# Optimization experiments

Hardware: AMD Instinct MI355X
Metric: run time of the kernel (lower is better)

Reference implementation:

```python
import jax, jax.numpy as jnp
import numpy as np

SCALE = 2
K_UP = 5
K_ENC = 3


def _conv(x, w, b, pad):
    # NCHW conv, OIHW weights
    y = jax.lax.conv_general_dilated(
        x, w, window_strides=(1, 1), padding=((pad, pad), (pad, pad)),
        dimension_numbers=('NCHW', 'OIHW', 'NCHW'))
    return y + b[None, :, None, None]


def setup_inputs() -> dict:
    key = jax.random.key(0)
    k0, k1, k2 = jax.random.split(key, 3)
    b, c, h, w = 4, 256, 64, 64
    c_mid = 64
    n_kernel = SCALE * SCALE * K_UP * K_UP  # 100
    x = jax.random.normal(k0, (b, c, h, w), jnp.float32)
    w1 = jax.random.normal(k1, (c_mid, c, K_ENC, K_ENC), jnp.float32) * 0.02
    b1 = jnp.zeros((c_mid,), jnp.float32)
    w2 = jax.random.normal(k2, (n_kernel, c_mid, 1, 1), jnp.float32) * 0.02
    b2 = jnp.zeros((n_kernel,), jnp.float32)
    return {"x": x, "w1": w1, "b1": b1, "w2": w2, "b2": b2}


def reference(x, w1, b1, w2, b2):
    b, c, h, w = x.shape
    s, k = SCALE, K_UP
    # kernel prediction encoder: 3x3 conv -> ReLU -> 1x1 conv
    feat = jax.nn.relu(_conv(x, w1, b1, K_ENC // 2))
    kern = _conv(feat, w2, b2, 0)                     # (b, s^2*k^2, h, w)
    kern = jax.nn.softmax(kern, axis=1)               # softmax over full channel dim (as in source)
    kern = kern.reshape(b, s * s, k * k, h, w)
    # F.unfold(x, k, padding=k//2) -> (b, c, k^2, h, w); torch ordering: kh major, kw minor
    pad = k // 2
    xp = jnp.pad(x, ((0, 0), (0, 0), (pad, pad), (pad, pad)))
    patches = jnp.stack([xp[:, :, i:i + h, j:j + w]
                         for i in range(k) for j in range(k)], axis=2)  # (b, c, k^2, h, w)
    # per-pixel weighted reassembly: sum over k^2 neighborhood
    out = jnp.einsum('bskhw,bckhw->bschw', kern, patches)  # (b, s^2, c, h, w)
    # view(b, s^2*c, h, w) then pixel_shuffle(scale), exactly matching torch semantics
    out = out.reshape(b, s * s * c, h, w)
    cout = (s * s * c) // (s * s)
    out = out.reshape(b, cout, s, s, h, w)
    out = out.transpose(0, 1, 4, 2, 5, 3).reshape(b, cout, h * s, w * s)
    return out
```

## Files before the change

### kernel.cpp

```cpp
#include <hip/hip_runtime.h>


#define BB 4
#define CC 256
#define HH 64
#define WW 64
#define CMID 64
#define NKCH 100

typedef __bf16 bf16;
typedef __bf16 bf16x8 __attribute__((ext_vector_type(8)));
typedef float f32x4 __attribute__((ext_vector_type(4)));

__device__ __forceinline__ void async_copy16(const void* gsrc, void* ldst) {
    __builtin_amdgcn_global_load_lds(
        (__attribute__((address_space(1))) void*)(void*)gsrc,
        (__attribute__((address_space(3))) void*)ldst, 16, 0, 0);
}

__global__ void k0a_transform(const float* __restrict__ w1, bf16* __restrict__ w1c) {
    int c8 = blockIdx.x;
    int oq = blockIdx.y;
    int tid = threadIdx.x;
    __shared__ __align__(16) float wf[16 * 300];

    for (int i = tid; i < 16 * 72; i += 256) {
        int o = i / 72, r = i % 72;
        *(float4*)&wf[o * 300 + r * 4] =
            *(const float4*)&w1[(size_t)(oq * 16 + o) * 2304 + c8 * 288 + r * 4];
    }
    __syncthreads();

    for (int t = tid; t < 576; t += 256) {
        int o = t & 15, q = (t >> 4) & 3, kk = t >> 6;
        union { bf16 h[8]; uint4 u; } v;
        #pragma unroll
        for (int i8 = 0; i8 < 8; ++i8)
            v.h[i8] = (bf16)wf[o * 300 + (q * 8 + i8) * 9 + kk];
        *(uint4*)&w1c[(size_t)((((c8 * 9 + kk) * 4 + q) * 64) + oq * 16 + o) * 8] = v.u;
    }
}

__global__ __launch_bounds__(512) void k12_fused(const float* __restrict__ x,
        const bf16* __restrict__ w1c, const float* __restrict__ b1,
        const float* __restrict__ w2, const float* __restrict__ b2,
        float* __restrict__ kern) {
    int bh = blockIdx.x;
    int b = bh >> 6, h = bh & 63;
    int tid = threadIdx.x;
    int lane = tid & 63, wid = tid >> 6;
    int l15 = lane & 15, quad = lane >> 4;
    int mhalf = wid & 1, nq = wid >> 1;

    __shared__ __align__(16) char smem[122112];
    bf16*  xs0  = (bf16*)smem;
    bf16*  xs1  = (bf16*)(smem + 15872);
    bf16*  wl0  = (bf16*)(smem + 31744);
    bf16*  wl1  = (bf16*)(smem + 68608);
    float* fs   = (float*)(smem + 105472);
    float* kts  = (float*)(smem + 31744);
    float* red  = (float*)smem;

    const float* xb = x + (size_t)b * (CC * HH * WW);

    int ppp[6], rrr[6];
    bool vmask[6];
    #pragma unroll
    for (int j = 0; j < 6; ++j) {
        int task = wid + j * 8;
        ppp[j] = task & 15;
        rrr[j] = task >> 4;
        int hr = h - 1 + rrr[j];
        vmask[j] = (hr >= 0 && hr < HH);
    }

    float fA0[6], fA1[6], fB0[6], fB1[6];
    #define LOADX(C8, F0, F1)                                                    \
        _Pragma("unroll")                                                        \
        for (int j = 0; j < 6; ++j) {                                            \
            if (vmask[j]) {                                                      \
                const float* src = xb + ((size_t)((C8) * 32 + 2 * ppp[j]) * (HH * WW)) \
                                 + (h - 1 + rrr[j]) * WW + lane;                 \
                F0[j] = src[0]; F1[j] = src[HH * WW];                            \
            }                                                                    \
        }
    #define WRITEB(F0, F1, XSDST)                                                \
        _Pragma("unroll")                                                        \
        for (int j = 0; j < 6; ++j) {                                            \
            if (vmask[j]) {                                                      \
                union { bf16 hh[2]; unsigned u; } cv;                            \
                cv.hh[0] = (bf16)F0[j]; cv.hh[1] = (bf16)F1[j];                  \
                *(unsigned*)&XSDST[(rrr[j] * 66 + 1 + lane) * 40 + 2 * ppp[j]] = cv.u; \
            }                                                                    \
        }
    #define ACOPY(C8, WDST)                                                      \
        for (int t = wid; t < 36; t += 8)                                        \
            async_copy16(w1c + ((((C8) * 36 + t) << 9) + lane * 8), (void*)&WDST[t << 9]);
    #define MFMAS(XSRC, WSRC)                                                    \
        _Pragma("unroll")                                                        \
        for (int kk = 0; kk < 9; ++kk) {                                         \
            int r3 = kk / 3, kw = kk % 3;                                        \
            bf16x8 a0 = *(const bf16x8*)&WSRC[((kk * 4 + quad) * 64 + mhalf * 32 + l15) * 8]; \
            bf16x8 a1 = *(const bf16x8*)&WSRC[((kk * 4 + quad) * 64 + mhalf * 32 + 16 + l15) * 8]; \
            bf16x8 xv = *(const bf16x8*)&XSRC[(r3 * 66 + nq * 16 + l15 + kw) * 40 + quad * 8]; \
            acc0 = __builtin_amdgcn_mfma_f32_16x16x32_bf16(a0, xv, acc0, 0, 0, 0); \
            acc1 = __builtin_amdgcn_mfma_f32_16x16x32_bf16(a1, xv, acc1, 0, 0, 0); \
        }

    for (int i = tid; i < 7936; i += 512) { xs0[i] = (bf16)0.f; xs1[i] = (bf16)0.f; }
    LOADX(0, fA0, fA1)
    ACOPY(0, wl0)
    __syncthreads();
    WRITEB(fA0, fA1, xs0)
    LOADX(1, fB0, fB1)
    __syncthreads();

    f32x4 acc0 = {0.f, 0.f, 0.f, 0.f}, acc1 = {0.f, 0.f, 0.f, 0.f};

    for (int c8 = 0; c8 < 8; c8 += 2) {
        ACOPY(c8 + 1, wl1)
        MFMAS(xs0, wl0)
        WRITEB(fB0, fB1, xs1)
        if (c8 < 6) { LOADX(c8 + 2, fA0, fA1) }
        __syncthreads();
        if (c8 < 6) { ACOPY(c8 + 2, wl0) }
        MFMAS(xs1, wl1)
        if (c8 < 6) { WRITEB(fA0, fA1, xs0) }
        if (c8 < 6) { LOADX(c8 + 3, fB0, fB1) }
        __syncthreads();
    }

    int px = nq * 16 + l15;
    #pragma unroll
    for (int mi = 0; mi < 2; ++mi) {
        int oc0 = mhalf * 32 + mi * 16 + quad * 4;
        float4 bv = *(const float4*)&b1[oc0];
        f32x4 v = mi ? acc1 : acc0;
        fs[(oc0 + 0) * 65 + px] = fmaxf(v[0] + bv.x, 0.f);
        fs[(oc0 + 1) * 65 + px] = fmaxf(v[1] + bv.y, 0.f);
        fs[(oc0 + 2) * 65 + px] = fmaxf(v[2] + bv.z, 0.f);
        fs[(oc0 + 3) * 65 + px] = fmaxf(v[3] + bv.w, 0.f);
    }
    __syncthreads();

    int w = lane;
    int g = wid, s2 = g & 3, ihalf = g >> 2;
    int i0 = ihalf ? 13 : 0;

    float4 fv[16];
    #pragma unroll
    for (int q = 0; q < 16; ++q) {
        fv[q].x = fs[(4 * q + 0) * 65 + w];
        fv[q].y = fs[(4 * q + 1) * 65 + w];
        fv[q].z = fs[(4 * q + 2) * 65 + w];
        fv[q].w = fs[(4 * q + 3) * 65 + w];
    }

    float lg[13];
    #pragma unroll
    for (int ii = 0; ii < 13; ++ii) {
        int idx = i0 + ii;
        bool act = (idx < 25);
        int oc = s2 * 25 + (act ? idx : 0);
        float a = b2[oc];
        const float4* wr = (const float4*)&w2[oc * 64];
        #pragma unroll
        for (int q = 0; q < 16; ++q) {
            float4 wv = wr[q];
            a += fv[q].x * wv.x + fv[q].y * wv.y + fv[q].z * wv.z + fv[q].w * wv.w;
        }
        lg[ii] = act ? a : -1e30f;
    }

    float m = -1e30f;
    #pragma unroll
    for (int ii = 0; ii < 13; ++ii) m = fmaxf(m, lg[ii]);
    red[g * 64 + w] = m;
    __syncthreads();
    m = fmaxf(fmaxf(fmaxf(red[0 * 64 + w], red[1 * 64 + w]),
                    fmaxf(red[2 * 64 + w], red[3 * 64 + w])),
              fmaxf(fmaxf(red[4 * 64 + w], red[5 * 64 + w]),
                    fmaxf(red[6 * 64 + w], red[7 * 64 + w])));
    float ssum = 0.f;
    #pragma unroll
    for (int ii = 0; ii < 13; ++ii) { lg[ii] = __expf(lg[ii] - m); ssum += lg[ii]; }
    red[512 + g * 64 + w] = ssum;
    __syncthreads();
    ssum = ((red[512 + 0 * 64 + w] + red[512 + 1 * 64 + w]) +
            (red[512 + 2 * 64 + w] + red[512 + 3 * 64 + w])) +
           ((red[512 + 4 * 64 + w] + red[512 + 5 * 64 + w]) +
            (red[512 + 6 * 64 + w] + red[512 + 7 * 64 + w]));
    float inv = 1.f / ssum;
    #pragma unroll
    for (int ii = 0; ii < 13; ++ii)
        if (i0 + ii < 25) kts[((i0 + ii) * 64 + w) * 4 + s2] = lg[ii] * inv;
    __syncthreads();

    float* kout = kern + (size_t)bh * 6400;
    for (int i = tid; i < 1600; i += 512)
        *(float4*)&kout[i * 4] = *(const float4*)&kts[i * 4];
    #undef LOADX
    #undef WRITEB
    #undef ACOPY
    #undef MFMAS
}

__global__ __launch_bounds__(256, 6) void k3_reassemble(const float* __restrict__ x,
        const float* __restrict__ kern, float* __restrict__ out) {
    int chunk = blockIdx.x;
    int bh = blockIdx.y;
    int b = bh >> 6, h = bh & 63;
    int tid = threadIdx.x;
    int w = tid & 63;
    int cg = tid >> 6;

    __shared__ __align__(16) float xs[5 * 4 * 68 * 4];

    #pragma unroll
    for (int k = 0; k < 5; ++k) {
        int idx = tid + k * 256;
        int u = idx & 15, cc = (idx >> 4) & 15, rr = idx >> 8;
        int hr = h - 2 + rr;
        float4 v = make_float4(0.f, 0.f, 0.f, 0.f);
        if (hr >= 0 && hr < HH)
            v = *(const float4*)&x[(((size_t)b * CC + chunk * 16 + cc) * HH + hr) * WW + 4 * u];
        int base = (rr * 4 + (cc >> 2)) * 68;
        int c = cc & 3;
        #pragma unroll
        for (int j = 0; j < 4; ++j) {
            int s = 2 + 4 * u + j;
            int sw = s ^ ((s >> 3) & 7);
            xs[(base + sw) * 4 + c] = ((const float*)&v)[j];
        }
    }
    for (int i = tid; i < 320; i += 256) {
        int c = i & 3;
        int q = (i >> 2) & 3;
        int rg = i >> 4;
        int slot = (q < 2) ? q : (q + 64);
        xs[(rg * 68 + slot) * 4 + c] = 0.f;
    }

    const float* kp = kern + (size_t)bh * 6400 + w * 4;
    f32x4 kv0[5];
    #pragma unroll
    for (int kw = 0; kw < 5; ++kw)
        kv0[kw] = *(const f32x4*)&kp[kw * 256];

    int swk[5];
    #pragma unroll
    for (int kw = 0; kw < 5; ++kw) {
        int s = w + kw;
        swk[kw] = s ^ ((s >> 3) & 7);
    }

    __syncthreads();

    f32x4 a0 = {0.f,0.f,0.f,0.f}, a1 = {0.f,0.f,0.f,0.f};
    f32x4 a2 = {0.f,0.f,0.f,0.f}, a3 = {0.f,0.f,0.f,0.f};
    #pragma unroll
    for (int r = 0; r < 5; ++r) {
        #pragma unroll
        for (int kw = 0; kw < 5; ++kw) {
            f32x4 kv = (r == 0) ? kv0[kw]
                                : *(const f32x4*)&kp[(r * 5 + kw) * 256];
            f32x4 xv = *(const f32x4*)&xs[((r * 4 + cg) * 68 + swk[kw]) * 4];
            a0 += kv.x * xv;
            a1 += kv.y * xv;
            a2 += kv.z * xv;
            a3 += kv.w * xv;
        }
    }

    int cq = chunk * 4 + cg;
    f32x4 accs[4] = {a0, a1, a2, a3};
    #pragma unroll
    for (int s = 0; s < 4; ++s) {
        size_t base = (((size_t)b * 256 + s * 64 + cq) * 128 + 2 * h) * 128 + 2 * w;
        *(float2*)&out[base]       = make_float2(accs[s][0], accs[s][1]);
        *(float2*)&out[base + 128] = make_float2(accs[s][2], accs[s][3]);
    }
}

extern "C" void kernel_launch(void* const* d_in, const int* in_sizes, int n_in,
                              void* d_out, int out_size, void* d_ws, size_t ws_size,
                              hipStream_t stream) {
    const float* x  = (const float*)d_in[0];
    const float* w1 = (const float*)d_in[1];
    const float* b1 = (const float*)d_in[2];
    const float* w2 = (const float*)d_in[3];
    const float* b2 = (const float*)d_in[4];
    float* out = (float*)d_out;

    char* wsb = (char*)d_ws;
    float* kern = (float*)wsb;
    bf16*  w1c  = (bf16*)(wsb + 6553600);

    k0a_transform<<<dim3(8, 4), 256, 0, stream>>>(w1, w1c);
    k12_fused<<<dim3(BB * HH), 512, 0, stream>>>(x, w1c, b1, w2, b2, kern);
    k3_reassemble<<<dim3(16, BB * HH), 256, 0, stream>>>(x, kern, out);
}
```

Before: 132.6 us.

## Fuse reassembly into encoder kernel, keeping softmax kernels in registers

Merges the reassembly stage into the encoder/softmax kernel. Each block now keeps its row's 100 softmax weights in registers from LDS instead of writing them to a global workspace and reading them back. The block then loops over 8 channel chunks, double-buffering x tiles in LDS while it computes. This removes a kernel launch and the workspace round trip. The cost is only 256 blocks of 512 threads handling all 256 channels, so parallelism and occupancy drop compared with the 4096-block reassembly grid.

```diff
diff --git a/kernel.cpp b/kernel.cpp
--- a/kernel.cpp
+++ b/kernel.cpp
@@ -41,10 +41,10 @@
     }
 }
 
-__global__ __launch_bounds__(512) void k12_fused(const float* __restrict__ x,
+__global__ __launch_bounds__(512) void k123_fused(const float* __restrict__ x,
         const bf16* __restrict__ w1c, const float* __restrict__ b1,
         const float* __restrict__ w2, const float* __restrict__ b2,
-        float* __restrict__ kern) {
+        float* __restrict__ out) {
     int bh = blockIdx.x;
     int b = bh >> 6, h = bh & 63;
     int tid = threadIdx.x;
@@ -58,7 +58,7 @@
     bf16*  wl0  = (bf16*)(smem + 31744);
     bf16*  wl1  = (bf16*)(smem + 68608);
     float* fs   = (float*)(smem + 105472);
-    float* kts  = (float*)(smem + 31744);
+    float* kts  = (float*)(smem + 68608);
     float* red  = (float*)smem;
 
     const float* xb = x + (size_t)b * (CC * HH * WW);
@@ -90,19 +90,19 @@
             if (vmask[j]) {                                                      \
                 union { bf16 hh[2]; unsigned u; } cv;                            \
                 cv.hh[0] = (bf16)F0[j]; cv.hh[1] = (bf16)F1[j];                  \
-                *(unsigned*)&XSDST[(rrr[j] * 66 + 1 + lane) * 40 + 2 * ppp[j]] = cv.u; \
+                *(unsigned*)&(XSDST)[(rrr[j] * 66 + 1 + lane) * 40 + 2 * ppp[j]] = cv.u; \
             }                                                                    \
         }
     #define ACOPY(C8, WDST)                                                      \
         for (int t = wid; t < 36; t += 8)                                        \
-            async_copy16(w1c + ((((C8) * 36 + t) << 9) + lane * 8), (void*)&WDST[t << 9]);
+            async_copy16(w1c + ((((C8) * 36 + t) << 9) + lane * 8), (void*)&(WDST)[t << 9]);
     #define MFMAS(XSRC, WSRC)                                                    \
         _Pragma("unroll")                                                        \
         for (int kk = 0; kk < 9; ++kk) {                                         \
             int r3 = kk / 3, kw = kk % 3;                                        \
-            bf16x8 a0 = *(const bf16x8*)&WSRC[((kk * 4 + quad) * 64 + mhalf * 32 + l15) * 8]; \
-            bf16x8 a1 = *(const bf16x8*)&WSRC[((kk * 4 + quad) * 64 + mhalf * 32 + 16 + l15) * 8]; \
-            bf16x8 xv = *(const bf16x8*)&XSRC[(r3 * 66 + nq * 16 + l15 + kw) * 40 + quad * 8]; \
+            bf16x8 a0 = *(const bf16x8*)&(WSRC)[((kk * 4 + quad) * 64 + mhalf * 32 + l15) * 8]; \
+            bf16x8 a1 = *(const bf16x8*)&(WSRC)[((kk * 4 + quad) * 64 + mhalf * 32 + 16 + l15) * 8]; \
+            bf16x8 xv = *(const bf16x8*)&(XSRC)[(r3 * 66 + nq * 16 + l15 + kw) * 40 + quad * 8]; \
             acc0 = __builtin_amdgcn_mfma_f32_16x16x32_bf16(a0, xv, acc0, 0, 0, 0); \
             acc1 = __builtin_amdgcn_mfma_f32_16x16x32_bf16(a1, xv, acc1, 0, 0, 0); \
         }
@@ -143,6 +143,35 @@
     }
     __syncthreads();
 
+    int t8 = tid & 255, h2 = tid >> 8;
+    int w3 = t8 & 63, cg3 = t8 >> 6;
+    #define XLOAD(P, V)                                                          \
+        _Pragma("unroll")                                                        \
+        for (int k = 0; k < 5; ++k) {                                            \
+            int idx = t8 + k * 256;                                              \
+            int u = idx & 15, cc = (idx >> 4) & 15, rr = idx >> 8;               \
+            int hr = h - 2 + rr;                                                 \
+            V[k] = make_float4(0.f, 0.f, 0.f, 0.f);                              \
+            if (hr >= 0 && hr < HH)                                              \
+                V[k] = *(const float4*)&x[(((size_t)b * CC + (2 * (P) + h2) * 16 + cc) * HH + hr) * WW + 4 * u]; \
+        }
+    #define XWRITE(V, TB)                                                        \
+        _Pragma("unroll")                                                        \
+        for (int k = 0; k < 5; ++k) {                                            \
+            int idx = t8 + k * 256;                                              \
+            int u = idx & 15, cc = (idx >> 4) & 15, rr = idx >> 8;               \
+            int bse = (rr * 4 + (cc >> 2)) * 68;                                 \
+            int c = cc & 3;                                                      \
+            _Pragma("unroll")                                                    \
+            for (int j = 0; j < 4; ++j) {                                        \
+                int s = 2 + 4 * u + j;                                           \
+                int sw = s ^ ((s >> 3) & 7);                                     \
+                (TB)[(bse + sw) * 4 + c] = ((const float*)&V[k])[j];             \
+            }                                                                    \
+        }
+    float4 xst[5];
+    XLOAD(0, xst)
+
     int w = lane;
     int g = wid, s2 = g & 3, ihalf = g >> 2;
     int i0 = ihalf ? 13 : 0;
@@ -196,90 +225,73 @@
         if (i0 + ii < 25) kts[((i0 + ii) * 64 + w) * 4 + s2] = lg[ii] * inv;
     __syncthreads();
 
-    float* kout = kern + (size_t)bh * 6400;
-    for (int i = tid; i < 1600; i += 512)
-        *(float4*)&kout[i * 4] = *(const float4*)&kts[i * 4];
+    f32x4 kv[5][5];
+    #pragma unroll
+    for (int r = 0; r < 5; ++r)
+        #pragma unroll
+        for (int kw = 0; kw < 5; ++kw)
+            kv[r][kw] = *(const f32x4*)&kts[((r * 5 + kw) * 64 + w3) * 4];
+
+    #pragma unroll
+    for (int reg = 0; reg < 4; ++reg) {
+        const int tb = (reg == 0) ? 0 : (reg == 1) ? 21760 : (reg == 2) ? 43520 : 94208;
+        if (tid < 320) {
+            int c = tid & 3, q = (tid >> 2) & 3, rg = tid >> 4;
+            int slot = (q < 2) ? q : (q + 64);
+            ((float*)(smem + tb))[(rg * 68 + slot) * 4 + c] = 0.f;
+        }
+    }
+
+    float* tb0 = (float*)(smem + (h2 ? 21760 : 0));
+    float* tb1 = (float*)(smem + (h2 ? 94208 : 43520));
+
+    int swk[5];
+    #pragma unroll
+    for (int kw = 0; kw < 5; ++kw) {
+        int s = w3 + kw;
+        swk[kw] = s ^ ((s >> 3) & 7);
+    }
+
+    XWRITE(xst, tb0)
+    __syncthreads();
+
+    for (int p = 0; p < 8; ++p) {
+        if (p < 7) { XLOAD(p + 1, xst) }
+        float* T = (p & 1) ? tb1 : tb0;
+        f32x4 a0 = {0.f,0.f,0.f,0.f}, a1 = {0.f,0.f,0.f,0.f};
+        f32x4 a2 = {0.f,0.f,0.f,0.f}, a3 = {0.f,0.f,0.f,0.f};
+        #pragma unroll
+        for (int r = 0; r < 5; ++r) {
+            #pragma unroll
+            for (int kw = 0; kw < 5; ++kw) {
+                f32x4 kvv = kv[r][kw];
+                f32x4 xv = *(const f32x4*)&T[((r * 4 + cg3) * 68 + swk[kw]) * 4];
+                a0 += kvv.x * xv;
+                a1 += kvv.y * xv;
+                a2 += kvv.z * xv;
+                a3 += kvv.w * xv;
+            }
+        }
+        int cq = (2 * p + h2) * 4 + cg3;
+        f32x4 accs[4] = {a0, a1, a2, a3};
+        #pragma unroll
+        for (int s = 0; s < 4; ++s) {
+            size_t base = (((size_t)b * 256 + s * 64 + cq) * 128 + 2 * h) * 128 + 2 * w3;
+            *(float2*)&out[base]       = make_float2(accs[s][0], accs[s][1]);
+            *(float2*)&out[base + 128] = make_float2(accs[s][2], accs[s][3]);
+        }
+        if (p < 7) {
+            float* Tnext = (p & 1) ? tb0 : tb1;
+            XWRITE(xst, Tnext)
+        }
+        __syncthreads();
+    }
     #undef LOADX
     #undef WRITEB
     #undef ACOPY
     #undef MFMAS
-}
-
-__global__ __launch_bounds__(256, 6) void k3_reassemble(const float* __restrict__ x,
-        const float* __restrict__ kern, float* __restrict__ out) {
-    int chunk = blockIdx.x;
-    int bh = blockIdx.y;
-    int b = bh >> 6, h = bh & 63;
-    int tid = threadIdx.x;
-    int w = tid & 63;
-    int cg = tid >> 6;
-
-    __shared__ __align__(16) float xs[5 * 4 * 68 * 4];
-
-    #pragma unroll
-    for (int k = 0; k < 5; ++k) {
-        int idx = tid + k * 256;
-        int u = idx & 15, cc = (idx >> 4) & 15, rr = idx >> 8;
-        int hr = h - 2 + rr;
-        float4 v = make_float4(0.f, 0.f, 0.f, 0.f);
-        if (hr >= 0 && hr < HH)
-            v = *(const float4*)&x[(((size_t)b * CC + chunk * 16 + cc) * HH + hr) * WW + 4 * u];
-        int base = (rr * 4 + (cc >> 2)) * 68;
-        int c = cc & 3;
-        #pragma unroll
-        for (int j = 0; j < 4; ++j) {
-            int s = 2 + 4 * u + j;
-            int sw = s ^ ((s >> 3) & 7);
-            xs[(base + sw) * 4 + c] = ((const float*)&v)[j];
-        }
-    }
-    for (int i = tid; i < 320; i += 256) {
-        int c = i & 3;
-        int q = (i >> 2) & 3;
-        int rg = i >> 4;
-        int slot = (q < 2) ? q : (q + 64);
-        xs[(rg * 68 + slot) * 4 + c] = 0.f;
-    }
-
-    const float* kp = kern + (size_t)bh * 6400 + w * 4;
-    f32x4 kv0[5];
-    #pragma unroll
-    for (int kw = 0; kw < 5; ++kw)
-        kv0[kw] = *(const f32x4*)&kp[kw * 256];
-
-    int swk[5];
-    #pragma unroll
-    for (int kw = 0; kw < 5; ++kw) {
-        int s = w + kw;
-        swk[kw] = s ^ ((s >> 3) & 7);
-    }
-
-    __syncthreads();
-
-    f32x4 a0 = {0.f,0.f,0.f,0.f}, a1 = {0.f,0.f,0.f,0.f};
-    f32x4 a2 = {0.f,0.f,0.f,0.f}, a3 = {0.f,0.f,0.f,0.f};
-    #pragma unroll
-    for (int r = 0; r < 5; ++r) {
-        #pragma unroll
-        for (int kw = 0; kw < 5; ++kw) {
-            f32x4 kv = (r == 0) ? kv0[kw]
-                                : *(const f32x4*)&kp[(r * 5 + kw) * 256];
-            f32x4 xv = *(const f32x4*)&xs[((r * 4 + cg) * 68 + swk[kw]) * 4];
-            a0 += kv.x * xv;
-            a1 += kv.y * xv;
-            a2 += kv.z * xv;
-            a3 += kv.w * xv;
-        }
-    }
-
-    int cq = chunk * 4 + cg;
-    f32x4 accs[4] = {a0, a1, a2, a3};
-    #pragma unroll
-    for (int s = 0; s < 4; ++s) {
-        size_t base = (((size_t)b * 256 + s * 64 + cq) * 128 + 2 * h) * 128 + 2 * w;
-        *(float2*)&out[base]       = make_float2(accs[s][0], accs[s][1]);
-        *(float2*)&out[base + 128] = make_float2(accs[s][2], accs[s][3]);
-    }
+    #undef XLOAD
+    #undef XWRITE
 }
 
 extern "C" void kernel_launch(void* const* d_in, const int* in_sizes, int n_in,
@@ -292,11 +304,8 @@
     const float* b2 = (const float*)d_in[4];
     float* out = (float*)d_out;
 
-    char* wsb = (char*)d_ws;
-    float* kern = (float*)wsb;
-    bf16*  w1c  = (bf16*)(wsb + 6553600);
+    bf16* w1c = (bf16*)d_ws;
 
     k0a_transform<<<dim3(8, 4), 256, 0, stream>>>(w1, w1c);
-    k12_fused<<<dim3(BB * HH), 512, 0, stream>>>(x, w1c, b1, w2, b2, kern);
-    k3_reassemble<<<dim3(16, BB * HH), 256, 0, stream>>>(x, kern, out);
+    k123_fused<<<dim3(BB * HH), 512, 0, stream>>>(x, w1c, b1, w2, b2, out);
 }
```

After: 402.5 us. 203% more time.
